# Kernel tuning notes

Hardware: AMD Instinct MI355X
Metric: run time of the kernel (lower is better)

Reference implementation:

```python
import jax, jax.numpy as jnp
import numpy as np

N_HEAD = 16
ROPE_BASE = 10000.0


def _rope_tables(T, head_dim, dtype):
    inv_freq = 1.0 / (ROPE_BASE ** (jnp.arange(0, head_dim, 2, dtype=jnp.float32) / head_dim))
    t = jnp.arange(T, dtype=jnp.float32)
    freqs = t[:, None] * inv_freq[None, :]          # [T, hd/2]
    emb = jnp.concatenate([freqs, freqs], axis=-1)  # [T, hd]
    return jnp.cos(emb).astype(dtype), jnp.sin(emb).astype(dtype)


def _rotate_half(x):
    h = x.shape[-1] // 2
    return jnp.concatenate([-x[..., h:], x[..., :h]], axis=-1)


def setup_inputs() -> dict:
    key = jax.random.key(0)
    k1, k2, k3 = jax.random.split(key, 3)
    B, T, C = 2, 2048, 1024
    x = jax.random.normal(k1, (B, T, C), dtype=jnp.float32)
    w_attn = jax.random.normal(k2, (3 * C, C), dtype=jnp.float32) * (1.0 / np.sqrt(C))
    w_proj = jax.random.normal(k3, (C, C), dtype=jnp.float32) * (1.0 / np.sqrt(C))
    return {"x": x, "w_attn": w_attn, "w_proj": w_proj}


def reference(x, w_attn, w_proj):
    B, T, C = x.shape
    H = N_HEAD
    hd = C // H

    qkv = jnp.einsum('btc,fc->btf', x, w_attn)          # [B,T,3C]
    q, k, v = jnp.split(qkv, 3, axis=-1)
    # [B,H,T,hd]
    q = q.reshape(B, T, H, hd).transpose(0, 2, 1, 3)
    k = k.reshape(B, T, H, hd).transpose(0, 2, 1, 3)
    v = v.reshape(B, T, H, hd).transpose(0, 2, 1, 3)

    cos, sin = _rope_tables(T, hd, x.dtype)             # [T,hd]
    cos = cos[None, None]
    sin = sin[None, None]
    q = q * cos + _rotate_half(q) * sin
    k = k * cos + _rotate_half(k) * sin

    scale = 1.0 / np.sqrt(hd)
    scores = jnp.einsum('bhqd,bhkd->bhqk', q, k) * scale  # [B,H,T,T]
    causal = jnp.tril(jnp.ones((T, T), dtype=bool))
    scores = jnp.where(causal[None, None], scores, jnp.finfo(scores.dtype).min)
    attn = jax.nn.softmax(scores, axis=-1)
    out = jnp.einsum('bhqk,bhkd->bhqd', attn, v)          # [B,H,T,hd]
    out = out.transpose(0, 2, 1, 3).reshape(B, T, C)
    return jnp.einsum('btc,oc->bto', out, w_proj)
```

## Files before the change

kernel.cpp:

```cpp
#include <hip/hip_runtime.h>
#include <hip/hip_bf16.h>
#include <stdint.h>

typedef unsigned short u16;
typedef __bf16 bf16x8 __attribute__((ext_vector_type(8)));
typedef float f32x4 __attribute__((ext_vector_type(4)));

#define B_ 2
#define T_ 2048
#define C_ 1024
#define H_ 16
#define HD 64
#define M_ (B_ * T_)
#define N3 (3 * C_)

__device__ __forceinline__ float bf2f(u16 u) {
  return __uint_as_float(((unsigned int)u) << 16);
}
__device__ __forceinline__ u16 f2bf(float f) {
  unsigned int u = __float_as_uint(f);
  u += 0x7FFF + ((u >> 16) & 1);
  return (u16)(u >> 16);
}

union U16x8 { uint4 v; u16 u[8]; };

__device__ __forceinline__ bf16x8 ldsAfrag(const char* base, int row, int kbyte) {
  int off = (row * 128 + kbyte) ^ ((row & 7) << 4);
  uint4 t = *reinterpret_cast<const uint4*>(base + off);
  return __builtin_bit_cast(bf16x8, t);
}
__device__ __forceinline__ bf16x8 ldsAfrag256(const char* base, int row, int kbyte) {
  int off = (row * 256 + kbyte) ^ ((row & 7) << 4);
  uint4 t = *reinterpret_cast<const uint4*>(base + off);
  return __builtin_bit_cast(bf16x8, t);
}

__global__ void cvt_bf16(const float* __restrict__ src, u16* __restrict__ dst, int n4) {
  int i = blockIdx.x * blockDim.x + threadIdx.x;
  int stride = gridDim.x * blockDim.x;
  for (; i < n4; i += stride) {
    float4 v = reinterpret_cast<const float4*>(src)[i];
    uint2 o;
    o.x = (unsigned)f2bf(v.x) | ((unsigned)f2bf(v.y) << 16);
    o.y = (unsigned)f2bf(v.z) | ((unsigned)f2bf(v.w) << 16);
    reinterpret_cast<uint2*>(dst)[i] = o;
  }
}

__global__ void rope_tables_kernel(float* __restrict__ cosT, float* __restrict__ sinT) {
  int t = blockIdx.x;
  int i = threadIdx.x;
  float inv = powf(10000.0f, -(float)i * (1.0f / 32.0f));
  float f = (float)t * inv;
  cosT[t * 32 + i] = cosf(f);
  sinT[t * 32 + i] = sinf(f);
}

template <bool OUT_F32>
__global__ __launch_bounds__(256) void gemm_bt(const u16* __restrict__ A,
                                               const u16* __restrict__ Bw,
                                               void* __restrict__ Cout,
                                               int M, int N, int K) {
  __shared__ uint4 ldsbuf[2048];
  char* As = (char*)ldsbuf;
  char* Bs = (char*)ldsbuf + 16384;
  const int tid = threadIdx.x;
  const int lane = tid & 63;
  const int wv = tid >> 6;
  const int wr = wv >> 1, wc = wv & 1;
  const int lrow = lane & 15, lgrp = lane >> 4;
  const long m0 = (long)blockIdx.x * 128, n0 = (long)blockIdx.y * 128;
  const int srow = tid >> 3, sc = tid & 7;
  f32x4 acc[4][4] = {};
  for (int k0 = 0; k0 < K; k0 += 64) {
    __syncthreads();
#pragma unroll
    for (int p = 0; p < 4; ++p) {
      int row = srow + p * 32;
      uint4 va = *reinterpret_cast<const uint4*>(A + (m0 + row) * K + k0 + sc * 8);
      *reinterpret_cast<uint4*>(As + ((row * 128 + sc * 16) ^ ((row & 7) << 4))) = va;
      uint4 vb = *reinterpret_cast<const uint4*>(Bw + (n0 + row) * K + k0 + sc * 8);
      *reinterpret_cast<uint4*>(Bs + ((row * 128 + sc * 16) ^ ((row & 7) << 4))) = vb;
    }
    __syncthreads();
#pragma unroll
    for (int ks = 0; ks < 2; ++ks) {
      bf16x8 af[4], bfr[4];
#pragma unroll
      for (int i = 0; i < 4; ++i) {
        af[i]  = ldsAfrag(As, wr * 64 + i * 16 + lrow, ks * 64 + lgrp * 16);
        bfr[i] = ldsAfrag(Bs, wc * 64 + i * 16 + lrow, ks * 64 + lgrp * 16);
      }
#pragma unroll
      for (int i = 0; i < 4; ++i)
#pragma unroll
        for (int j = 0; j < 4; ++j)
          acc[i][j] = __builtin_amdgcn_mfma_f32_16x16x32_bf16(af[i], bfr[j], acc[i][j], 0, 0, 0);
    }
  }
#pragma unroll
  for (int i = 0; i < 4; ++i)
#pragma unroll
    for (int j = 0; j < 4; ++j) {
      long r0 = m0 + wr * 64 + i * 16 + lgrp * 4;
      long c  = n0 + wc * 64 + j * 16 + lrow;
#pragma unroll
      for (int r = 0; r < 4; ++r) {
        float v = acc[i][j][r];
        if (OUT_F32)
          ((float*)Cout)[(r0 + r) * N + c] = v;
        else
          ((u16*)Cout)[(r0 + r) * N + c] = f2bf(v);
      }
    }
}

__global__ __launch_bounds__(256) void rope_reshape(const u16* __restrict__ qkv,
                                                    const float* __restrict__ cosT,
                                                    const float* __restrict__ sinT,
                                                    u16* __restrict__ Q,
                                                    u16* __restrict__ K,
                                                    u16* __restrict__ Vt) {
  __shared__ u16 Vs[64][80];
  const int tid = threadIdx.x;
  const int tblk = blockIdx.x, bh = blockIdx.y;
  const int b = bh >> 4, h = bh & 15;
  const int tl = tid >> 2, quar = tid & 3;
  const int t = tblk * 64 + tl;
  const u16* rowp = qkv + ((size_t)(b * T_ + t)) * N3 + h * HD;
  const int d0 = quar * 8;
  float cs[8], sn[8];
#pragma unroll
  for (int j = 0; j < 8; ++j) {
    cs[j] = cosT[t * 32 + d0 + j];
    sn[j] = sinT[t * 32 + d0 + j];
  }
#pragma unroll
  for (int part = 0; part < 2; ++part) {
    const u16* p = rowp + part * C_;
    U16x8 x1, x2, o1, o2;
    x1.v = *reinterpret_cast<const uint4*>(p + d0);
    x2.v = *reinterpret_cast<const uint4*>(p + d0 + 32);
#pragma unroll
    for (int j = 0; j < 8; ++j) {
      float a = bf2f(x1.u[j]), c2 = bf2f(x2.u[j]);
      o1.u[j] = f2bf(a * cs[j] - c2 * sn[j]);
      o2.u[j] = f2bf(c2 * cs[j] + a * sn[j]);
    }
    u16* dst = (part ? K : Q) + ((size_t)bh * T_ + t) * HD;
    *reinterpret_cast<uint4*>(dst + d0) = o1.v;
    *reinterpret_cast<uint4*>(dst + d0 + 32) = o2.v;
  }
  const u16* pv = rowp + 2 * C_;
#pragma unroll
  for (int c = 0; c < 2; ++c) {
    int d = quar * 16 + c * 8;
    *reinterpret_cast<uint4*>(&Vs[tl][d]) = *reinterpret_cast<const uint4*>(pv + d);
  }
  __syncthreads();
  const int d = tid >> 2, tq = tid & 3;
  U16x8 a, bv;
#pragma unroll
  for (int j = 0; j < 8; ++j) a.u[j] = Vs[tq * 16 + j][d];
#pragma unroll
  for (int j = 0; j < 8; ++j) bv.u[j] = Vs[tq * 16 + 8 + j][d];
  u16* dstv = Vt + ((size_t)bh * HD + d) * T_ + tblk * 64 + tq * 16;
  *reinterpret_cast<uint4*>(dstv) = a.v;
  *reinterpret_cast<uint4*>(dstv + 8) = bv.v;
}

__global__ __launch_bounds__(256) void attn_fwd2(const u16* __restrict__ Q,
                                                 const u16* __restrict__ K,
                                                 const u16* __restrict__ Vt,
                                                 u16* __restrict__ O) {
  __shared__ char lds[49152];
  char* Ks = lds;
  char* Vs = lds + 16384;
  const int tid = threadIdx.x;
  const int lane = tid & 63, wv = tid >> 6;
  const int lrow = lane & 15, lgrp = lane >> 4;
  char* Ps = lds + 32768 + wv * 4096;
  const int bh = blockIdx.y;
  const int b = bh >> 4, h = bh & 15;
  const u16* Qh = Q + (size_t)bh * T_ * HD;
  const u16* Kh = K + (size_t)bh * T_ * HD;
  const u16* Vh = Vt + (size_t)bh * HD * T_;
  const int krow = tid >> 3, kcol = tid & 7;
  const int vd = tid >> 4, vkc = tid & 15;

#pragma unroll
  for (int uu = 0; uu < 2; ++uu) {
    const int unit = uu ? (31 - (int)blockIdx.x) : (int)blockIdx.x;
    const int qs = unit * 64;
    bf16x8 qf[2];
#pragma unroll
    for (int ks = 0; ks < 2; ++ks) {
      uint4 t4 = *reinterpret_cast<const uint4*>(
          Qh + (size_t)(qs + wv * 16 + lrow) * HD + ks * 32 + lgrp * 8);
      qf[ks] = __builtin_bit_cast(bf16x8, t4);
    }
    f32x4 o[4] = {};
    float mrun[4], lrun[4];
#pragma unroll
    for (int r = 0; r < 4; ++r) { mrun[r] = -__builtin_inff(); lrun[r] = 0.f; }

    const int niter = (unit >> 1) + 1;
    for (int kt = 0; kt < niter; ++kt) {
      const int k0 = kt * 128;
      __syncthreads();
      {
#pragma unroll
        for (int p = 0; p < 4; ++p) {
          int row = krow + p * 32;
          uint4 v = *reinterpret_cast<const uint4*>(Kh + (size_t)(k0 + row) * HD + kcol * 8);
          *reinterpret_cast<uint4*>(Ks + ((row * 128 + kcol * 16) ^ ((row & 7) << 4))) = v;
        }
#pragma unroll
        for (int p = 0; p < 4; ++p) {
          int d = vd + p * 16;
          uint4 v = *reinterpret_cast<const uint4*>(Vh + (size_t)d * T_ + k0 + vkc * 8);
          *reinterpret_cast<uint4*>(Vs + ((d * 256 + vkc * 16) ^ ((d & 7) << 4))) = v;
        }
      }
      __syncthreads();

      f32x4 s[8] = {};
      __builtin_amdgcn_s_setprio(1);
#pragma unroll
      for (int ks = 0; ks < 2; ++ks)
#pragma unroll
        for (int n = 0; n < 8; ++n) {
          bf16x8 bk = ldsAfrag(Ks, n * 16 + lrow, ks * 64 + lgrp * 16);
          s[n] = __builtin_amdgcn_mfma_f32_16x16x32_bf16(qf[ks], bk, s[n], 0, 0, 0);
        }
      __builtin_amdgcn_s_setprio(0);

      const bool diag = (kt == niter - 1);
#pragma unroll
      for (int n = 0; n < 8; ++n)
#pragma unroll
        for (int r = 0; r < 4; ++r) {
          float v = s[n][r] * 0.125f;
          if (diag) {
            int kg = k0 + n * 16 + lrow;
            int qg = qs + wv * 16 + lgrp * 4 + r;
            v = (kg <= qg) ? v : -__builtin_inff();
          }
          s[n][r] = v;
        }

#pragma unroll
      for (int r = 0; r < 4; ++r) {
        float tm = s[0][r];
#pragma unroll
        for (int n = 1; n < 8; ++n) tm = fmaxf(tm, s[n][r]);
#pragma unroll
        for (int msk = 1; msk < 16; msk <<= 1) tm = fmaxf(tm, __shfl_xor(tm, msk, 64));
        float nm = fmaxf(mrun[r], tm);
        float alpha = __expf(mrun[r] - nm);
        mrun[r] = nm;
        float psum = 0.f;
#pragma unroll
        for (int n = 0; n < 8; ++n) {
          float p = __expf(s[n][r] - nm);
          s[n][r] = p;
          psum += p;
        }
#pragma unroll
        for (int msk = 1; msk < 16; msk <<= 1) psum += __shfl_xor(psum, msk, 64);
        lrun[r] = lrun[r] * alpha + psum;
#pragma unroll
        for (int dn = 0; dn < 4; ++dn) o[dn][r] *= alpha;
      }

#pragma unroll
      for (int n = 0; n < 8; ++n)
#pragma unroll
        for (int r = 0; r < 4; ++r) {
          int prow = lgrp * 4 + r;
          int off = (prow * 256 + (n * 16 + lrow) * 2) ^ ((prow & 7) << 4);
          *reinterpret_cast<u16*>(Ps + off) = f2bf(s[n][r]);
        }

      __builtin_amdgcn_s_setprio(1);
#pragma unroll
      for (int ks = 0; ks < 4; ++ks) {
        bf16x8 pa = ldsAfrag256(Ps, lrow, ks * 64 + lgrp * 16);
#pragma unroll
        for (int dn = 0; dn < 4; ++dn) {
          bf16x8 bv = ldsAfrag256(Vs, dn * 16 + lrow, ks * 64 + lgrp * 16);
          o[dn] = __builtin_amdgcn_mfma_f32_16x16x32_bf16(pa, bv, o[dn], 0, 0, 0);
        }
      }
      __builtin_amdgcn_s_setprio(0);
    }

#pragma unroll
    for (int r = 0; r < 4; ++r) {
      float inv = 1.0f / lrun[r];
      int t = qs + wv * 16 + lgrp * 4 + r;
#pragma unroll
      for (int dn = 0; dn < 4; ++dn) {
        int c = h * HD + dn * 16 + lrow;
        O[((size_t)(b * T_ + t)) * C_ + c] = f2bf(o[dn][r] * inv);
      }
    }
  }
}

extern "C" void kernel_launch(void* const* d_in, const int* in_sizes, int n_in,
                              void* d_out, int out_size, void* d_ws, size_t ws_size,
                              hipStream_t stream) {
  const float* x  = (const float*)d_in[0];
  const float* wa = (const float*)d_in[1];
  const float* wp = (const float*)d_in[2];
  float* out = (float*)d_out;
  char* ws = (char*)d_ws;
  size_t off = 0;
  auto alloc = [&](size_t bytes) {
    char* p = ws + off;
    off += (bytes + 255) & ~(size_t)255;
    return p;
  };
  u16* xb   = (u16*)alloc((size_t)M_ * C_ * 2);
  u16* wab  = (u16*)alloc((size_t)N3 * C_ * 2);
  u16* wpb  = (u16*)alloc((size_t)C_ * C_ * 2);
  u16* qkvb = (u16*)alloc((size_t)M_ * N3 * 2);
  u16* Qb   = (u16*)alloc((size_t)B_ * H_ * T_ * HD * 2);
  u16* Kb   = (u16*)alloc((size_t)B_ * H_ * T_ * HD * 2);
  u16* Vtb  = (u16*)alloc((size_t)B_ * H_ * T_ * HD * 2);
  u16* Ob   = (u16*)alloc((size_t)M_ * C_ * 2);
  float* cosT = (float*)alloc((size_t)T_ * 32 * 4);
  float* sinT = (float*)alloc((size_t)T_ * 32 * 4);
  (void)in_sizes; (void)n_in; (void)out_size; (void)ws_size;

  cvt_bf16<<<1024, 256, 0, stream>>>(x, xb, M_ * C_ / 4);
  cvt_bf16<<<1024, 256, 0, stream>>>(wa, wab, N3 * C_ / 4);
  cvt_bf16<<<512, 256, 0, stream>>>(wp, wpb, C_ * C_ / 4);
  rope_tables_kernel<<<T_, 32, 0, stream>>>(cosT, sinT);
  gemm_bt<false><<<dim3(M_ / 128, N3 / 128), 256, 0, stream>>>(xb, wab, qkvb, M_, N3, C_);
  rope_reshape<<<dim3(T_ / 64, B_ * H_), 256, 0, stream>>>(qkvb, cosT, sinT, Qb, Kb, Vtb);
  attn_fwd2<<<dim3(16, B_ * H_), 256, 0, stream>>>(Qb, Kb, Vtb, Ob);
  gemm_bt<true><<<dim3(M_ / 128, C_ / 128), 256, 0, stream>>>(Ob, wpb, out, M_, C_, C_);
}
```

Measured before the change: 145.1 us.

## Prefetch K/V tiles into registers and transpose S to simplify softmax

```diff
diff --git a/kernel.cpp b/kernel.cpp
--- a/kernel.cpp
+++ b/kernel.cpp
@@ -170,17 +170,17 @@
   *reinterpret_cast<uint4*>(dstv + 8) = bv.v;
 }
 
-__global__ __launch_bounds__(256) void attn_fwd2(const u16* __restrict__ Q,
+__global__ __launch_bounds__(256) void attn_fwd3(const u16* __restrict__ Q,
                                                  const u16* __restrict__ K,
                                                  const u16* __restrict__ Vt,
                                                  u16* __restrict__ O) {
-  __shared__ char lds[49152];
-  char* Ks = lds;
-  char* Vs = lds + 16384;
+  __shared__ uint4 lds4[3072];
+  char* Ks = (char*)lds4;
+  char* Vs = (char*)lds4 + 16384;
   const int tid = threadIdx.x;
   const int lane = tid & 63, wv = tid >> 6;
   const int lrow = lane & 15, lgrp = lane >> 4;
-  char* Ps = lds + 32768 + wv * 4096;
+  char* Ps = (char*)lds4 + 32768 + wv * 4096;
   const int bh = blockIdx.y;
   const int b = bh >> 4, h = bh & 15;
   const u16* Qh = Q + (size_t)bh * T_ * HD;
@@ -193,6 +193,7 @@
   for (int uu = 0; uu < 2; ++uu) {
     const int unit = uu ? (31 - (int)blockIdx.x) : (int)blockIdx.x;
     const int qs = unit * 64;
+    const int q_glob = qs + wv * 16 + lrow;
     bf16x8 qf[2];
 #pragma unroll
     for (int ks = 0; ks < 2; ++ks) {
@@ -201,29 +202,34 @@
       qf[ks] = __builtin_bit_cast(bf16x8, t4);
     }
     f32x4 o[4] = {};
-    float mrun[4], lrun[4];
-#pragma unroll
-    for (int r = 0; r < 4; ++r) { mrun[r] = -__builtin_inff(); lrun[r] = 0.f; }
+    float mrun = -__builtin_inff(), lrun = 0.f;
 
     const int niter = (unit >> 1) + 1;
+    uint4 kreg[4], vreg[4];
+#pragma unroll
+    for (int p = 0; p < 4; ++p) {
+      kreg[p] = *reinterpret_cast<const uint4*>(Kh + (size_t)(krow + p * 32) * HD + kcol * 8);
+      vreg[p] = *reinterpret_cast<const uint4*>(Vh + (size_t)(vd + p * 16) * T_ + vkc * 8);
+    }
+
     for (int kt = 0; kt < niter; ++kt) {
       const int k0 = kt * 128;
+#pragma unroll
+      for (int p = 0; p < 4; ++p) {
+        int row = krow + p * 32;
+        *reinterpret_cast<uint4*>(Ks + ((row * 128 + kcol * 16) ^ ((row & 7) << 4))) = kreg[p];
+        int d = vd + p * 16;
+        *reinterpret_cast<uint4*>(Vs + ((d * 256 + vkc * 16) ^ ((d & 7) << 4))) = vreg[p];
+      }
       __syncthreads();
-      {
+      if (kt + 1 < niter) {
+        const int k1 = k0 + 128;
 #pragma unroll
         for (int p = 0; p < 4; ++p) {
-          int row = krow + p * 32;
-          uint4 v = *reinterpret_cast<const uint4*>(Kh + (size_t)(k0 + row) * HD + kcol * 8);
-          *reinterpret_cast<uint4*>(Ks + ((row * 128 + kcol * 16) ^ ((row & 7) << 4))) = v;
-        }
-#pragma unroll
-        for (int p = 0; p < 4; ++p) {
-          int d = vd + p * 16;
-          uint4 v = *reinterpret_cast<const uint4*>(Vh + (size_t)d * T_ + k0 + vkc * 8);
-          *reinterpret_cast<uint4*>(Vs + ((d * 256 + vkc * 16) ^ ((d & 7) << 4))) = v;
-        }
-      }
-      __syncthreads();
+          kreg[p] = *reinterpret_cast<const uint4*>(Kh + (size_t)(k1 + krow + p * 32) * HD + kcol * 8);
+          vreg[p] = *reinterpret_cast<const uint4*>(Vh + (size_t)(vd + p * 16) * T_ + k1 + vkc * 8);
+        }
+      }
 
       f32x4 s[8] = {};
       __builtin_amdgcn_s_setprio(1);
@@ -232,7 +238,7 @@
 #pragma unroll
         for (int n = 0; n < 8; ++n) {
           bf16x8 bk = ldsAfrag(Ks, n * 16 + lrow, ks * 64 + lgrp * 16);
-          s[n] = __builtin_amdgcn_mfma_f32_16x16x32_bf16(qf[ks], bk, s[n], 0, 0, 0);
+          s[n] = __builtin_amdgcn_mfma_f32_16x16x32_bf16(bk, qf[ks], s[n], 0, 0, 0);
         }
       __builtin_amdgcn_s_setprio(0);
 
@@ -243,45 +249,54 @@
         for (int r = 0; r < 4; ++r) {
           float v = s[n][r] * 0.125f;
           if (diag) {
-            int kg = k0 + n * 16 + lrow;
-            int qg = qs + wv * 16 + lgrp * 4 + r;
-            v = (kg <= qg) ? v : -__builtin_inff();
+            int kg = k0 + n * 16 + lgrp * 4 + r;
+            v = (kg <= q_glob) ? v : -__builtin_inff();
           }
           s[n][r] = v;
         }
 
-#pragma unroll
-      for (int r = 0; r < 4; ++r) {
-        float tm = s[0][r];
-#pragma unroll
-        for (int n = 1; n < 8; ++n) tm = fmaxf(tm, s[n][r]);
-#pragma unroll
-        for (int msk = 1; msk < 16; msk <<= 1) tm = fmaxf(tm, __shfl_xor(tm, msk, 64));
-        float nm = fmaxf(mrun[r], tm);
-        float alpha = __expf(mrun[r] - nm);
-        mrun[r] = nm;
-        float psum = 0.f;
-#pragma unroll
-        for (int n = 0; n < 8; ++n) {
-          float p = __expf(s[n][r] - nm);
-          s[n][r] = p;
-          psum += p;
-        }
-#pragma unroll
-        for (int msk = 1; msk < 16; msk <<= 1) psum += __shfl_xor(psum, msk, 64);
-        lrun[r] = lrun[r] * alpha + psum;
-#pragma unroll
-        for (int dn = 0; dn < 4; ++dn) o[dn][r] *= alpha;
-      }
-
-#pragma unroll
-      for (int n = 0; n < 8; ++n)
+      float tm = fmaxf(fmaxf(s[0][0], s[0][1]), fmaxf(s[0][2], s[0][3]));
+#pragma unroll
+      for (int n = 1; n < 8; ++n)
+        tm = fmaxf(tm, fmaxf(fmaxf(s[n][0], s[n][1]), fmaxf(s[n][2], s[n][3])));
+      tm = fmaxf(tm, __shfl_xor(tm, 16, 64));
+      tm = fmaxf(tm, __shfl_xor(tm, 32, 64));
+      if (!__all(tm <= mrun + 8.f)) {
+        float nm = fmaxf(mrun, tm);
+        float alpha = __expf(mrun - nm);
+        mrun = nm;
+        lrun *= alpha;
 #pragma unroll
         for (int r = 0; r < 4; ++r) {
-          int prow = lgrp * 4 + r;
-          int off = (prow * 256 + (n * 16 + lrow) * 2) ^ ((prow & 7) << 4);
-          *reinterpret_cast<u16*>(Ps + off) = f2bf(s[n][r]);
-        }
+          float ao = __shfl(alpha, lgrp * 4 + r, 64);
+#pragma unroll
+          for (int dn = 0; dn < 4; ++dn) o[dn][r] *= ao;
+        }
+      }
+      float ps0 = 0.f, ps1 = 0.f;
+#pragma unroll
+      for (int n = 0; n < 8; ++n) {
+        float p0 = __expf(s[n][0] - mrun);
+        float p1 = __expf(s[n][1] - mrun);
+        float p2 = __expf(s[n][2] - mrun);
+        float p3 = __expf(s[n][3] - mrun);
+        s[n][0] = p0; s[n][1] = p1; s[n][2] = p2; s[n][3] = p3;
+        ps0 += p0 + p1;
+        ps1 += p2 + p3;
+      }
+      float psum = ps0 + ps1;
+      psum += __shfl_xor(psum, 16, 64);
+      psum += __shfl_xor(psum, 32, 64);
+      lrun += psum;
+
+#pragma unroll
+      for (int n = 0; n < 8; ++n) {
+        uint2 w;
+        w.x = (unsigned)f2bf(s[n][0]) | ((unsigned)f2bf(s[n][1]) << 16);
+        w.y = (unsigned)f2bf(s[n][2]) | ((unsigned)f2bf(s[n][3]) << 16);
+        int off = (lrow * 256 + n * 32 + lgrp * 8) ^ ((lrow & 7) << 4);
+        *reinterpret_cast<uint2*>(Ps + off) = w;
+      }
 
       __builtin_amdgcn_s_setprio(1);
 #pragma unroll
@@ -294,11 +309,12 @@
         }
       }
       __builtin_amdgcn_s_setprio(0);
+      __syncthreads();
     }
 
 #pragma unroll
     for (int r = 0; r < 4; ++r) {
-      float inv = 1.0f / lrun[r];
+      float inv = 1.0f / __shfl(lrun, lgrp * 4 + r, 64);
       int t = qs + wv * 16 + lgrp * 4 + r;
 #pragma unroll
       for (int dn = 0; dn < 4; ++dn) {
@@ -341,6 +357,6 @@
   rope_tables_kernel<<<T_, 32, 0, stream>>>(cosT, sinT);
   gemm_bt<false><<<dim3(M_ / 128, N3 / 128), 256, 0, stream>>>(xb, wab, qkvb, M_, N3, C_);
   rope_reshape<<<dim3(T_ / 64, B_ * H_), 256, 0, stream>>>(qkvb, cosT, sinT, Qb, Kb, Vtb);
-  attn_fwd2<<<dim3(16, B_ * H_), 256, 0, stream>>>(Qb, Kb, Vtb, Ob);
+  attn_fwd3<<<dim3(16, B_ * H_), 256, 0, stream>>>(Qb, Kb, Vtb, Ob);
   gemm_bt<true><<<dim3(M_ / 128, C_ / 128), 256, 0, stream>>>(Ob, wpb, out, M_, C_, C_);
 }
```

New measurement: 187.3 us. 29.1% more time.
